# Kernel tuning notes

Measured on AMD Instinct MI355X. Metric: run time of the kernel, lower is better.

The kernel has to match this reference:

```python
import jax, jax.numpy as jnp
import numpy as np

NEG_SLOPE = 0.01  # nn.LeakyReLU default
NUM_GRAPHS = 64


def leaky_relu(x):
    return jnp.where(x >= 0, x, NEG_SLOPE * x)


def gcn_conv(x, edge_index, W, b):
    """PyG GCNConv: add self-loops, symmetric norm, aggregate, + bias."""
    n = x.shape[0]
    h = x @ W  # [N, F]
    loop = jnp.arange(n, dtype=edge_index.dtype)
    src = jnp.concatenate([edge_index[0], loop])
    dst = jnp.concatenate([edge_index[1], loop])
    deg = jax.ops.segment_sum(jnp.ones_like(dst, dtype=h.dtype), dst, num_segments=n)
    dinv = jnp.where(deg > 0, deg ** -0.5, 0.0)
    norm = dinv[src] * dinv[dst]  # [E+N]
    msg = h[src] * norm[:, None]  # [E+N, F] dominant intermediate
    out = jax.ops.segment_sum(msg, dst, num_segments=n)
    return out + b


def gep(x, batch, num_graphs):
    """global mean pool over batch segment ids."""
    s = jax.ops.segment_sum(x, batch, num_segments=num_graphs)
    cnt = jax.ops.segment_sum(jnp.ones(x.shape[0], dtype=x.dtype), batch, num_segments=num_graphs)
    return s / jnp.maximum(cnt, 1.0)[:, None]


def setup_inputs() -> dict:
    key = jax.random.key(0)
    ks = jax.random.split(key, 16)
    N, E, F, D, B = 10000, 80000, 1024, 128, NUM_GRAPHS
    sc = 1.0 / np.sqrt(F)
    inp = {
        "pro1_x": jax.random.normal(ks[0], (N, F), jnp.float32),
        "pro1_edge_index": jax.random.randint(ks[1], (2, E), 0, N, jnp.int64),
        "pro1_batch": jnp.sort(jax.random.randint(ks[2], (N,), 0, B, jnp.int64)),
        "pro2_x": jax.random.normal(ks[3], (N, F), jnp.float32),
        "pro2_edge_index": jax.random.randint(ks[4], (2, E), 0, N, jnp.int64),
        "pro2_batch": jnp.sort(jax.random.randint(ks[5], (N,), 0, B, jnp.int64)),
        "mas1_straight": 0, "mas1_flipped": 0, "mas2_straight": 0, "mas2_flipped": 0,
        "conv1_W": jax.random.normal(ks[6], (F, F), jnp.float32) * sc,
        "conv1_b": jnp.zeros((F,), jnp.float32),
        "fc1_W": jax.random.normal(ks[7], (F, D), jnp.float32) * sc,
        "fc1_b": jnp.zeros((D,), jnp.float32),
        "conv2_W": jax.random.normal(ks[8], (F, F), jnp.float32) * sc,
        "conv2_b": jnp.zeros((F,), jnp.float32),
        "fc2_W": jax.random.normal(ks[9], (F, D), jnp.float32) * sc,
        "fc2_b": jnp.zeros((D,), jnp.float32),
        "final_W": jax.random.normal(ks[10], (2 * D, 1), jnp.float32) * (1.0 / np.sqrt(2 * D)),
        "final_b": jnp.zeros((1,), jnp.float32),
    }
    return inp


def reference(pro1_x, pro1_edge_index, pro1_batch, pro2_x, pro2_edge_index, pro2_batch,
              mas1_straight, mas1_flipped, mas2_straight, mas2_flipped,
              conv1_W, conv1_b, fc1_W, fc1_b, conv2_W, conv2_b, fc2_W, fc2_b,
              final_W, final_b):
    # branch 1 (dropout = identity at inference)
    x = leaky_relu(gcn_conv(pro1_x, pro1_edge_index, conv1_W, conv1_b))
    x = gep(x, pro1_batch, NUM_GRAPHS)
    x = leaky_relu(x @ fc1_W + fc1_b)
    # branch 2
    xt = leaky_relu(gcn_conv(pro2_x, pro2_edge_index, conv2_W, conv2_b))
    xt = gep(xt, pro2_batch, NUM_GRAPHS)
    xt = leaky_relu(xt @ fc2_W + fc2_b)
    combined = jnp.concatenate([x, xt], axis=1)  # [B, 256]
    return combined @ final_W + final_b  # [B, 1]
```

## Files before the change

### kernel.cpp

```cpp
#include <hip/hip_runtime.h>
#include <cstdint>
#include <cstddef>

#define FDIM 1024
#define DDIM 128
#define NGRAPH 64
#define CHUNKS 16

#define AS1 __attribute__((address_space(1)))
#define AS3 __attribute__((address_space(3)))

typedef float f32x4 __attribute__((ext_vector_type(4)));
typedef short s16x8 __attribute__((ext_vector_type(8)));

__device__ __forceinline__ unsigned short f2bf(float f) {
  unsigned int x = __float_as_uint(f);
  unsigned int r = (x + 0x7fffu + ((x >> 16) & 1u)) >> 16;
  return (unsigned short)r;
}
__device__ __forceinline__ float bf2f(unsigned short u) {
  return __uint_as_float(((unsigned int)u) << 16);
}

__device__ __forceinline__ int lower_bound(const int* a, int n, int v) {
  int lo = 0, hi = n;
  while (lo < hi) {
    int mid = (lo + hi) >> 1;
    if (a[mid] < v) lo = mid + 1; else hi = mid;
  }
  return lo;
}
__global__ __launch_bounds__(256) void k_init_cnt(float4* pool1, float4* pool2,
                                                  int* deg1, int* deg2,
                                                  const int* __restrict__ batch1,
                                                  const int* __restrict__ batch2,
                                                  int* cnt1, int* gstart1,
                                                  int* cnt2, int* gstart2, int N) {
  int bid = blockIdx.x, t = threadIdx.x;
  const float4 z = make_float4(0.f, 0.f, 0.f, 0.f);
  if (bid < 64) {
    pool1[bid * 256 + t] = z;
  } else if (bid < 128) {
    pool2[(bid - 64) * 256 + t] = z;
  } else if (bid < 168) {
    int i = (bid - 128) * 256 + t;
    if (i < N) deg1[i] = 1;
  } else if (bid < 208) {
    int i = (bid - 168) * 256 + t;
    if (i < N) deg2[i] = 1;
  } else {
    if (t < 128) {
      const int* batch = (t < NGRAPH) ? batch1 : batch2;
      int* cnt = (t < NGRAPH) ? cnt1 : cnt2;
      int* gstart = (t < NGRAPH) ? gstart1 : gstart2;
      int g = t & (NGRAPH - 1);
      int lo = lower_bound(batch, N, g);
      int hi = lower_bound(batch, N, g + 1);
      gstart[g] = lo;
      cnt[g] = hi - lo;
    }
  }
}

__global__ void k_prep(const int* __restrict__ ei1, const int* __restrict__ ei2,
                       int* deg1, int* deg2, int E) {
  const int* ei = blockIdx.y ? ei2 : ei1;
  int* deg = blockIdx.y ? deg2 : deg1;
  int i = blockIdx.x * blockDim.x + threadIdx.x;
  if (i < E) atomicAdd(&deg[ei[E + i]], 1);
}

#define SCAN_T 1024
#define SCAN_PER 16
__global__ __launch_bounds__(SCAN_T) void k_scan(const int* __restrict__ deg1,
                                                 const int* __restrict__ deg2,
                                                 int* off1, int* off2,
                                                 int* cur1, int* cur2,
                                                 float* dinv1, float* dinv2, int n) {
  const int* deg = blockIdx.x ? deg2 : deg1;
  int* off = blockIdx.x ? off2 : off1;
  int* cur = blockIdx.x ? cur2 : cur1;
  float* dinv = blockIdx.x ? dinv2 : dinv1;
  __shared__ int sums[SCAN_T];
  int t = threadIdx.x;
  int base = t * SCAN_PER;
  int local[SCAN_PER];
  int s = 0;
  #pragma unroll
  for (int i = 0; i < SCAN_PER; ++i) {
    int idx = base + i;
    int d = (idx < n) ? deg[idx] : 0;
    local[i] = s;
    s += d;
    if (idx < n) dinv[idx] = rsqrtf((float)d);
  }
  sums[t] = s;
  __syncthreads();
  for (int o = 1; o < SCAN_T; o <<= 1) {
    int v = (t >= o) ? sums[t - o] : 0;
    __syncthreads();
    sums[t] += v;
    __syncthreads();
  }
  int basesum = (t > 0) ? sums[t - 1] : 0;
  #pragma unroll
  for (int i = 0; i < SCAN_PER; ++i) {
    int idx = base + i;
    if (idx < n) { int o = basesum + local[i]; off[idx] = o; cur[idx] = o; }
  }
  if (t == SCAN_T - 1) off[n] = sums[SCAN_T - 1];
}

__global__ void k_fill(const int* __restrict__ ei1, const int* __restrict__ ei2,
                       int* cur1, int* cur2,
                       const float* __restrict__ dinv1, const float* __restrict__ dinv2,
                       int* adjsrc1, int* adjsrc2,
                       float* adjw1, float* adjw2, int E, int N) {
  const int* ei = blockIdx.y ? ei2 : ei1;
  int* cur = blockIdx.y ? cur2 : cur1;
  const float* dinv = blockIdx.y ? dinv2 : dinv1;
  int* adjsrc = blockIdx.y ? adjsrc2 : adjsrc1;
  float* adjw = blockIdx.y ? adjw2 : adjw1;
  int i = blockIdx.x * blockDim.x + threadIdx.x;
  if (i < E) {
    int s = ei[i];
    int d = ei[E + i];
    int p = atomicAdd(&cur[d], 1);
    adjsrc[p] = s;
    adjw[p] = dinv[s] * dinv[d];
  }
  if (i < N) {
    int p = atomicAdd(&cur[i], 1);
    adjsrc[p] = i;
    adjw[p] = dinv[i] * dinv[i];
  }
}

__global__ __launch_bounds__(256) void k_cast(const float4* __restrict__ x1,
                                              const float4* __restrict__ x2,
                                              const float* __restrict__ W1,
                                              const float* __restrict__ W2,
                                              ushort4* xb1, ushort4* xb2,
                                              unsigned short* Wt1, unsigned short* Wt2,
                                              int n4, int nxb) {
  __shared__ unsigned short tile[64][65];
  int bid = blockIdx.x, t = threadIdx.x;
  if (bid < 2 * nxb) {
    int br = bid >= nxb;
    const float4* x = br ? x2 : x1;
    ushort4* xb = br ? xb2 : xb1;
    int i = (bid - br * nxb) * 256 + t;
    if (i < n4) {
      float4 v = x[i];
      ushort4 o;
      o.x = f2bf(v.x); o.y = f2bf(v.y); o.z = f2bf(v.z); o.w = f2bf(v.w);
      xb[i] = o;
    }
  } else {
    int w = bid - 2 * nxb;
    int br = w >= 256;
    const float* W = br ? W2 : W1;
    unsigned short* Wt = br ? Wt2 : Wt1;
    int tid16 = w - br * 256;
    int kb = tid16 >> 4, nb = tid16 & 15;
    int tn = t & 63, tg = t >> 6;
    #pragma unroll
    for (int r = 0; r < 16; ++r) {
      int kk = tg * 16 + r;
      tile[kk][tn] = f2bf(W[(size_t)(kb * 64 + kk) * FDIM + nb * 64 + tn]);
    }
    __syncthreads();
    #pragma unroll
    for (int r = 0; r < 16; ++r) {
      int nn = tg * 16 + r;
      Wt[(size_t)(nb * 64 + nn) * FDIM + kb * 64 + tn] = tile[tn][nn];
    }
  }
}

__global__ __launch_bounds__(256) void k_gemm_bf16(const unsigned short* __restrict__ A1,
                                                   const unsigned short* __restrict__ A2,
                                                   const unsigned short* __restrict__ B1,
                                                   const unsigned short* __restrict__ B2,
                                                   unsigned short* __restrict__ C1,
                                                   unsigned short* __restrict__ C2,
                                                   int M) {
  const unsigned short* A = blockIdx.y ? A2 : A1;
  const unsigned short* Bt = blockIdx.y ? B2 : B1;
  unsigned short* C = blockIdx.y ? C2 : C1;
  const int K = FDIM;
  __shared__ unsigned short sm[8192];
  int tid = threadIdx.x;
  int w = tid >> 6, lane = tid & 63;
  int wm = w >> 1, wn = w & 1;

  int per_xcd = gridDim.x >> 3;
  int l = (blockIdx.x & 7) * per_xcd + (blockIdx.x >> 3);
  int m0 = (l >> 3) * 128;
  int n0 = (l & 7) * 128;

  int sub = lane >> 2;
  int kq = lane & 3;

  f32x4 acc[4][4];
  #pragma unroll
  for (int i = 0; i < 4; ++i)
    #pragma unroll
    for (int j = 0; j < 4; ++j)
      acc[i][j] = (f32x4){0.f, 0.f, 0.f, 0.f};

  for (int k0 = 0; k0 < K; k0 += 32) {
    #pragma unroll
    for (int j = 0; j < 2; ++j) {
      int chunk = w * 2 + j;
      int ra = m0 + chunk * 16 + sub;
      if (ra > M - 1) ra = M - 1;
      const unsigned short* ga = A + (size_t)ra * K + k0 + kq * 8;
      __builtin_amdgcn_global_load_lds((const AS1 unsigned int*)ga,
                                       (AS3 unsigned int*)&sm[chunk * 512], 16, 0, 0);
      int rb = n0 + chunk * 16 + sub;
      const unsigned short* gb = Bt + (size_t)rb * K + k0 + kq * 8;
      __builtin_amdgcn_global_load_lds((const AS1 unsigned int*)gb,
                                       (AS3 unsigned int*)&sm[4096 + chunk * 512], 16, 0, 0);
    }
    __syncthreads();
    s16x8 af[4], bfr[4];
    #pragma unroll
    for (int i = 0; i < 4; ++i) {
      int rowa = wm * 64 + i * 16 + (lane & 15);
      af[i] = *(const s16x8*)&sm[rowa * 32 + (lane >> 4) * 8];
      int rowb = wn * 64 + i * 16 + (lane & 15);
      bfr[i] = *(const s16x8*)&sm[4096 + rowb * 32 + (lane >> 4) * 8];
    }
    #pragma unroll
    for (int i = 0; i < 4; ++i)
      #pragma unroll
      for (int j = 0; j < 4; ++j)
        acc[i][j] = __builtin_amdgcn_mfma_f32_16x16x32_bf16(af[i], bfr[j], acc[i][j], 0, 0, 0);
    __syncthreads();
  }

  #pragma unroll
  for (int i = 0; i < 4; ++i) {
    int row_base = m0 + wm * 64 + i * 16 + (lane >> 4) * 4;
    #pragma unroll
    for (int j = 0; j < 4; ++j) {
      int col = n0 + wn * 64 + j * 16 + (lane & 15);
      #pragma unroll
      for (int r = 0; r < 4; ++r) {
        int row = row_base + r;
        if (row < M) C[(size_t)row * FDIM + col] = f2bf(acc[i][j][r]);
      }
    }
  }
}

__global__ __launch_bounds__(256) void k_aggpool(const unsigned short* __restrict__ h1,
                                                 const unsigned short* __restrict__ h2,
                                                 const int* __restrict__ off1,
                                                 const int* __restrict__ off2,
                                                 const int* __restrict__ adjsrc1,
                                                 const int* __restrict__ adjsrc2,
                                                 const float* __restrict__ adjw1,
                                                 const float* __restrict__ adjw2,
                                                 const float* __restrict__ bias1,
                                                 const float* __restrict__ bias2,
                                                 const int* __restrict__ cnt1,
                                                 const int* __restrict__ cnt2,
                                                 const int* __restrict__ gstart1,
                                                 const int* __restrict__ gstart2,
                                                 float* pool1, float* pool2) {
  int br = blockIdx.z;
  const unsigned short* h = br ? h2 : h1;
  const int* off = br ? off2 : off1;
  const int* adjsrc = br ? adjsrc2 : adjsrc1;
  const float* adjw = br ? adjw2 : adjw1;
  const float* bias = br ? bias2 : bias1;
  const int* cnt = br ? cnt2 : cnt1;
  const int* gstart = br ? gstart2 : gstart1;
  float* pool = br ? pool2 : pool1;

  int g = blockIdx.x, q = blockIdx.y;
  int t = threadIdx.x;
  int n = cnt[g];
  int start = gstart[g];
  int per = (n + CHUNKS - 1) / CHUNKS;
  int v0 = start + q * per;
  int v1 = min(start + n, v0 + per);
  if (v0 >= v1) return;

  float4 b4 = ((const float4*)bias)[t];
  float s0 = 0.f, s1 = 0.f, s2 = 0.f, s3 = 0.f;
  for (int v = v0; v < v1; ++v) {
    int pb = off[v], pe = off[v + 1];
    float a0 = 0.f, a1 = 0.f, a2 = 0.f, a3 = 0.f;
    for (int p = pb; p < pe; ++p) {
      int sidx = adjsrc[p];
      float wgt = adjw[p];
      ushort4 hv = ((const ushort4*)(h + (size_t)sidx * FDIM))[t];
      a0 += wgt * bf2f(hv.x); a1 += wgt * bf2f(hv.y);
      a2 += wgt * bf2f(hv.z); a3 += wgt * bf2f(hv.w);
    }
    a0 += b4.x; a1 += b4.y; a2 += b4.z; a3 += b4.w;
    s0 += (a0 >= 0.f) ? a0 : 0.01f * a0;
    s1 += (a1 >= 0.f) ? a1 : 0.01f * a1;
    s2 += (a2 >= 0.f) ? a2 : 0.01f * a2;
    s3 += (a3 >= 0.f) ? a3 : 0.01f * a3;
  }
  float ic = 1.0f / fmaxf((float)n, 1.0f);
  float* pg = pool + (size_t)g * FDIM + t * 4;
  atomicAdd(pg + 0, s0 * ic);
  atomicAdd(pg + 1, s1 * ic);
  atomicAdd(pg + 2, s2 * ic);
  atomicAdd(pg + 3, s3 * ic);
}

__global__ __launch_bounds__(DDIM) void k_fc(const float* __restrict__ pool1,
                                             const float* __restrict__ pool2,
                                             const float* __restrict__ W1,
                                             const float* __restrict__ W2,
                                             const float* __restrict__ b1,
                                             const float* __restrict__ b2,
                                             float* out1, float* out2) {
  const float* pool = blockIdx.y ? pool2 : pool1;
  const float* W = blockIdx.y ? W2 : W1;
  const float* b = blockIdx.y ? b2 : b1;
  float* out = blockIdx.y ? out2 : out1;
  int g = blockIdx.x;
  int j = threadIdx.x;
  __shared__ float xs[FDIM];
  for (int k = j; k < FDIM; k += DDIM) xs[k] = pool[(size_t)g * FDIM + k];
  __syncthreads();
  float acc = b[j];
  for (int k = 0; k < FDIM; ++k) acc += xs[k] * W[(size_t)k * DDIM + j];
  out[g * DDIM + j] = (acc >= 0.f) ? acc : 0.01f * acc;
}

__global__ __launch_bounds__(DDIM) void k_final(const float* __restrict__ o1,
                                                const float* __restrict__ o2,
                                                const float* __restrict__ W,
                                                const float* __restrict__ b,
                                                float* __restrict__ out) {
  int g = blockIdx.x;
  int t = threadIdx.x;
  float acc = o1[g * DDIM + t] * W[t] + o2[g * DDIM + t] * W[DDIM + t];
  #pragma unroll
  for (int o = 32; o > 0; o >>= 1) acc += __shfl_down(acc, o);
  __shared__ float ws2[2];
  if ((t & 63) == 0) ws2[t >> 6] = acc;
  __syncthreads();
  if (t == 0) out[g] = ws2[0] + ws2[1] + b[0];
}

extern "C" void kernel_launch(void* const* d_in, const int* in_sizes, int n_in,
                              void* d_out, int out_size, void* d_ws, size_t ws_size,
                              hipStream_t stream) {
  const float* x1 = (const float*)d_in[0];
  const int* ei1 = (const int*)d_in[1];
  const int* batch1 = (const int*)d_in[2];
  const float* x2 = (const float*)d_in[3];
  const int* ei2 = (const int*)d_in[4];
  const int* batch2 = (const int*)d_in[5];
  const float* conv1_W = (const float*)d_in[10];
  const float* conv1_b = (const float*)d_in[11];
  const float* fc1_W = (const float*)d_in[12];
  const float* fc1_b = (const float*)d_in[13];
  const float* conv2_W = (const float*)d_in[14];
  const float* conv2_b = (const float*)d_in[15];
  const float* fc2_W = (const float*)d_in[16];
  const float* fc2_b = (const float*)d_in[17];
  const float* final_W = (const float*)d_in[18];
  const float* final_b = (const float*)d_in[19];
  float* out = (float*)d_out;

  const int N = in_sizes[2];
  const int E = in_sizes[1] / 2;
  const int A = E + N;

  size_t off_b = 0;
  auto alloc = [&](size_t bytes) -> void* {
    void* p = (char*)d_ws + off_b;
    off_b += (bytes + 255) & ~(size_t)255;
    return p;
  };
  unsigned short* xbf1 = (unsigned short*)alloc((size_t)N * FDIM * 2);
  unsigned short* xbf2 = (unsigned short*)alloc((size_t)N * FDIM * 2);
  unsigned short* hbf1 = (unsigned short*)alloc((size_t)N * FDIM * 2);
  unsigned short* hbf2 = (unsigned short*)alloc((size_t)N * FDIM * 2);
  unsigned short* Wt1 = (unsigned short*)alloc((size_t)FDIM * FDIM * 2);
  unsigned short* Wt2 = (unsigned short*)alloc((size_t)FDIM * FDIM * 2);
  int* deg1 = (int*)alloc(N * 4);
  int* deg2 = (int*)alloc(N * 4);
  int* cnt1 = (int*)alloc(NGRAPH * 4);
  int* cnt2 = (int*)alloc(NGRAPH * 4);
  int* gstart1 = (int*)alloc(NGRAPH * 4);
  int* gstart2 = (int*)alloc(NGRAPH * 4);
  int* off1 = (int*)alloc((N + 1) * 4);
  int* off2 = (int*)alloc((N + 1) * 4);
  int* cur1 = (int*)alloc(N * 4);
  int* cur2 = (int*)alloc(N * 4);
  float* dinv1 = (float*)alloc(N * 4);
  float* dinv2 = (float*)alloc(N * 4);
  int* adjsrc1 = (int*)alloc((size_t)A * 4);
  int* adjsrc2 = (int*)alloc((size_t)A * 4);
  float* adjw1 = (float*)alloc((size_t)A * 4);
  float* adjw2 = (float*)alloc((size_t)A * 4);
  float* pool1 = (float*)alloc(NGRAPH * FDIM * 4);
  float* pool2 = (float*)alloc(NGRAPH * FDIM * 4);
  float* fco1 = (float*)alloc(NGRAPH * DDIM * 4);
  float* fco2 = (float*)alloc(NGRAPH * DDIM * 4);

  const int T = 256;
  int gE = (E + T - 1) / T;
  int n4 = N * FDIM / 4;
  int nxb = (n4 + T - 1) / T;
  int mt = (N + 127) / 128;
  dim3 gGemm(mt * 8, 2);
  dim3 gPrep(gE, 2);
  dim3 gAgg(NGRAPH, CHUNKS, 2);
  dim3 gFc(NGRAPH, 2);

  k_init_cnt<<<209, T, 0, stream>>>((float4*)pool1, (float4*)pool2, deg1, deg2,
                                    batch1, batch2, cnt1, gstart1, cnt2, gstart2, N);
  k_prep<<<gPrep, T, 0, stream>>>(ei1, ei2, deg1, deg2, E);
  k_scan<<<2, SCAN_T, 0, stream>>>(deg1, deg2, off1, off2, cur1, cur2, dinv1, dinv2, N);
  k_fill<<<gPrep, T, 0, stream>>>(ei1, ei2, cur1, cur2, dinv1, dinv2,
                                  adjsrc1, adjsrc2, adjw1, adjw2, E, N);
  k_cast<<<2 * nxb + 512, T, 0, stream>>>((const float4*)x1, (const float4*)x2,
                                          conv1_W, conv2_W,
                                          (ushort4*)xbf1, (ushort4*)xbf2, Wt1, Wt2,
                                          n4, nxb);
  k_gemm_bf16<<<gGemm, 256, 0, stream>>>(xbf1, xbf2, Wt1, Wt2, hbf1, hbf2, N);
  k_aggpool<<<gAgg, 256, 0, stream>>>(hbf1, hbf2, off1, off2, adjsrc1, adjsrc2,
                                      adjw1, adjw2, conv1_b, conv2_b,
                                      cnt1, cnt2, gstart1, gstart2, pool1, pool2);
  k_fc<<<gFc, DDIM, 0, stream>>>(pool1, pool2, fc1_W, fc2_W, fc1_b, fc2_b, fco1, fco2);
  k_final<<<NGRAPH, DDIM, 0, stream>>>(fco1, fco2, final_W, final_b, out);
}
```

Measured before the change: 365.6 us.

## Split aggregation by feature column chunks with wave-per-node parallelism

Restructures the aggregate+pool kernel so each block handles a 128-column feature slice and four wavefronts process different nodes concurrently. Partial sums are then reduced through shared memory before one atomic per column. Consecutive block indices share a graph and node range across the eight column chunks, which aims to improve cache locality of gathered rows and increase memory-level parallelism. In exchange each lane issues narrower 4-byte loads, and adjacency data is read once per column chunk.

Result: slower. 397.2 us (+8.6%).

```diff
diff --git a/kernel.cpp b/kernel.cpp
--- a/kernel.cpp
+++ b/kernel.cpp
@@ -5,7 +5,8 @@
 #define FDIM 1024
 #define DDIM 128
 #define NGRAPH 64
-#define CHUNKS 16
+#define FCH 8
+#define QN 4
 
 #define AS1 __attribute__((address_space(1)))
 #define AS3 __attribute__((address_space(3)))
@@ -270,7 +271,7 @@
                                                  const int* __restrict__ gstart1,
                                                  const int* __restrict__ gstart2,
                                                  float* pool1, float* pool2) {
-  int br = blockIdx.z;
+  int br = blockIdx.y;
   const unsigned short* h = br ? h2 : h1;
   const int* off = br ? off2 : off1;
   const int* adjsrc = br ? adjsrc2 : adjsrc1;
@@ -280,39 +281,49 @@
   const int* gstart = br ? gstart2 : gstart1;
   float* pool = br ? pool2 : pool1;
 
-  int g = blockIdx.x, q = blockIdx.y;
+  int x = blockIdx.x;
+  int chunk = x & (FCH - 1);
+  int r = x >> 3;
+  int g = r & (NGRAPH - 1);
+  int q = r >> 6;
+
   int t = threadIdx.x;
+  int grp = t >> 6, lane = t & 63;
+
   int n = cnt[g];
   int start = gstart[g];
-  int per = (n + CHUNKS - 1) / CHUNKS;
+  int per = (n + QN - 1) / QN;
   int v0 = start + q * per;
   int v1 = min(start + n, v0 + per);
-  if (v0 >= v1) return;
-
-  float4 b4 = ((const float4*)bias)[t];
-  float s0 = 0.f, s1 = 0.f, s2 = 0.f, s3 = 0.f;
-  for (int v = v0; v < v1; ++v) {
+
+  int colbase = chunk * 128 + lane * 2;
+  float2 b2 = *(const float2*)(bias + colbase);
+  float s0 = 0.f, s1 = 0.f;
+
+  for (int v = v0 + grp; v < v1; v += 4) {
     int pb = off[v], pe = off[v + 1];
-    float a0 = 0.f, a1 = 0.f, a2 = 0.f, a3 = 0.f;
+    float a0 = 0.f, a1 = 0.f;
     for (int p = pb; p < pe; ++p) {
       int sidx = adjsrc[p];
       float wgt = adjw[p];
-      ushort4 hv = ((const ushort4*)(h + (size_t)sidx * FDIM))[t];
-      a0 += wgt * bf2f(hv.x); a1 += wgt * bf2f(hv.y);
-      a2 += wgt * bf2f(hv.z); a3 += wgt * bf2f(hv.w);
-    }
-    a0 += b4.x; a1 += b4.y; a2 += b4.z; a3 += b4.w;
+      unsigned int hv = *(const unsigned int*)(h + (size_t)sidx * FDIM + colbase);
+      a0 += wgt * bf2f((unsigned short)(hv & 0xffff));
+      a1 += wgt * bf2f((unsigned short)(hv >> 16));
+    }
+    a0 += b2.x; a1 += b2.y;
     s0 += (a0 >= 0.f) ? a0 : 0.01f * a0;
     s1 += (a1 >= 0.f) ? a1 : 0.01f * a1;
-    s2 += (a2 >= 0.f) ? a2 : 0.01f * a2;
-    s3 += (a3 >= 0.f) ? a3 : 0.01f * a3;
-  }
-  float ic = 1.0f / fmaxf((float)n, 1.0f);
-  float* pg = pool + (size_t)g * FDIM + t * 4;
-  atomicAdd(pg + 0, s0 * ic);
-  atomicAdd(pg + 1, s1 * ic);
-  atomicAdd(pg + 2, s2 * ic);
-  atomicAdd(pg + 3, s3 * ic);
+  }
+
+  __shared__ float sm[4][128];
+  sm[grp][lane * 2] = s0;
+  sm[grp][lane * 2 + 1] = s1;
+  __syncthreads();
+  if (t < 128) {
+    float sum = sm[0][t] + sm[1][t] + sm[2][t] + sm[3][t];
+    float ic = 1.0f / fmaxf((float)n, 1.0f);
+    atomicAdd(pool + (size_t)g * FDIM + chunk * 128 + t, sum * ic);
+  }
 }
 
 __global__ __launch_bounds__(DDIM) void k_fc(const float* __restrict__ pool1,
@@ -417,7 +428,7 @@
   int mt = (N + 127) / 128;
   dim3 gGemm(mt * 8, 2);
   dim3 gPrep(gE, 2);
-  dim3 gAgg(NGRAPH, CHUNKS, 2);
+  dim3 gAgg(FCH * NGRAPH * QN, 2);
   dim3 gFc(NGRAPH, 2);
 
   k_init_cnt<<<209, T, 0, stream>>>((float4*)pool1, (float4*)pool2, deg1, deg2,
```
